# Kernel tuning notes

Measured on AMD Instinct MI355X. Metric: run time of the kernel, lower is better.

## Reference

```python
import jax, jax.numpy as jnp
import numpy as np

H = 7        # num attention heads (must divide D=791)
TOP_NUM = 2  # hard-coded in select(attn_tensor, 2)


def setup_inputs() -> dict:
    key = jax.random.key(0)
    ks = jax.random.split(key, 7)
    B, N, D = 32, 512, 791  # D = 2*hidden_dim + 23, hidden_dim=384
    s = 1.0 / np.sqrt(D)
    return {
        "fuse_feature": jax.random.normal(ks[0], (B, N, D), jnp.float32),
        "Wq": jax.random.normal(ks[1], (D, D), jnp.float32) * s,
        "bq": jax.random.normal(ks[2], (D,), jnp.float32) * 0.01,
        "Wk": jax.random.normal(ks[3], (D, D), jnp.float32) * s,
        "bk": jax.random.normal(ks[4], (D,), jnp.float32) * 0.01,
        "W_gc": jax.random.normal(ks[5], (D, D), jnp.float32) * s,
        "b_gc": jax.random.normal(ks[6], (D,), jnp.float32) * 0.01,
    }


def _select(mat, top_num):
    """Faithful jax version of select(): per-batch top-k threshold,
    symmetrize (mask + mask^T), then fill diagonal with 1."""
    B, N, _ = mat.shape
    flat = mat.reshape(B, N * N)
    kth = jax.lax.top_k(flat, top_num)[0][:, -1]          # [B]
    m = (flat >= kth[:, None]).astype(mat.dtype).reshape(B, N, N)
    adj = m + jnp.swapaxes(m, -2, -1)                     # values in {0,1,2}
    eye = jnp.eye(N, dtype=bool)
    return jnp.where(eye[None], jnp.asarray(1.0, mat.dtype), adj)


def reference(fuse_feature, Wq, bq, Wk, bk, W_gc, b_gc):
    B, N, D = fuse_feature.shape
    dk = D // H

    # score_mask: positions where fuse @ fuse^T == 0 (padding detector)
    gram = jnp.einsum("bnd,bmd->bnm", fuse_feature, fuse_feature)
    score_mask = (gram == 0)[:, None]                     # [B,1,N,N]

    # multi-head attention probabilities (eval mode: no dropout)
    q = (fuse_feature @ Wq + bq).reshape(B, N, H, dk).transpose(0, 2, 1, 3)
    k = (fuse_feature @ Wk + bk).reshape(B, N, H, dk).transpose(0, 2, 1, 3)
    scores = jnp.einsum("bhnd,bhmd->bhnm", q, k) / jnp.sqrt(jnp.asarray(dk, q.dtype))
    scores = jnp.where(score_mask, -1e9, scores)
    valid = (~score_mask[..., 0:1]).astype(scores.dtype)  # [B,1,N,1]
    p_attn = jax.nn.softmax(scores, axis=-1) * valid

    attn = p_attn.sum(axis=1)                             # [B,N,N]
    att_adj = _select(attn, TOP_NUM) * attn

    # GraphConvolution (kg_gc): adj @ (x W) / (rowsum(adj)+1) + b, then relu
    hidden = fuse_feature @ W_gc
    denom = att_adj.sum(axis=2, keepdims=True) + 1.0
    out = jnp.einsum("bnm,bmd->bnd", att_adj, hidden) / denom + b_gc
    return jax.nn.relu(out)
```

## Files before the change

kernel.cpp:

```cpp
#include <hip/hip_runtime.h>

#define B_  32
#define N_  512
#define D_  791
#define H_  7
#define DK_ 113
#define M_  (B_*N_)
#define KP_ 800
#define DP_ 896
#define NKT 25

typedef __attribute__((ext_vector_type(8))) short bf16x8;
typedef __attribute__((ext_vector_type(4))) float f32x4;

__device__ __forceinline__ ushort f2bf_rn(float x) {
    uint u = __float_as_uint(x);
    uint r = (u + 0x7FFFu + ((u >> 16) & 1u)) >> 16;
    return (ushort)r;
}
__device__ __forceinline__ float bf2f(ushort h) {
    return __uint_as_float(((uint)h) << 16);
}
__device__ __forceinline__ void split_bf16(float x, ushort& h, ushort& l) {
    h = f2bf_rn(x);
    l = f2bf_rn(x - bf2f(h));
}

__device__ __forceinline__ void gload16(const void* g, void* l) {
    __builtin_amdgcn_global_load_lds(
        (const __attribute__((address_space(1))) void*)g,
        (__attribute__((address_space(3))) void*)l, 16, 0, 0);
}

__global__ __launch_bounds__(256)
void splitX_kernel(const float* __restrict__ X, ushort* __restrict__ Xh,
                   ushort* __restrict__ Xl)
{
    int g = blockIdx.x * 256 + threadIdx.x;
    if (g >= M_ * 100) return;
    int row = g / 100, grp = g % 100;
    int k0 = grp * 8;
    float v[8];
    if (k0 + 8 <= D_) {
        const float* p = X + (size_t)row * D_ + k0;
        #pragma unroll
        for (int i = 0; i < 8; ++i) v[i] = p[i];
    } else {
        #pragma unroll
        for (int i = 0; i < 8; ++i) {
            int k = k0 + i;
            v[i] = (k < D_) ? X[(size_t)row * D_ + k] : 0.f;
        }
    }
    bf16x8 hv, lv;
    #pragma unroll
    for (int i = 0; i < 8; ++i) {
        ushort h, l; split_bf16(v[i], h, l);
        hv[i] = (short)h; lv[i] = (short)l;
    }
    *(bf16x8*)&Xh[(size_t)row * KP_ + k0] = hv;
    *(bf16x8*)&Xl[(size_t)row * KP_ + k0] = lv;
}

__global__ __launch_bounds__(256)
void castWt_kernel(const float* __restrict__ W0, const float* __restrict__ W1,
                   const float* __restrict__ W2,
                   ushort* __restrict__ B0h, ushort* __restrict__ B0l,
                   ushort* __restrict__ B1h, ushort* __restrict__ B1l,
                   ushort* __restrict__ B2h, ushort* __restrict__ B2l)
{
    __shared__ ushort WsH[32][34], WsL[32][34];
    const int pc0 = blockIdx.x * 32;
    const int k0  = blockIdx.y * 32;
    const int w   = blockIdx.z;
    const float* W = (w == 0) ? W0 : (w == 1) ? W1 : W2;
    ushort* Bh = (w == 0) ? B0h : (w == 1) ? B1h : B2h;
    ushort* Bl = (w == 0) ? B0l : (w == 1) ? B1l : B2l;
    const int tx = threadIdx.x & 31, ty = threadIdx.x >> 5;

    #pragma unroll
    for (int r = 0; r < 4; ++r) {
        int kl = ty + 8 * r, k = k0 + kl;
        int pc = pc0 + tx;
        int src;
        if (w == 2) src = (pc < D_) ? pc : -1;
        else { int hh = pc >> 7, off = pc & 127; src = (off < DK_) ? hh * DK_ + off : -1; }
        float v = (src >= 0 && k < D_) ? W[(size_t)k * D_ + src] : 0.f;
        ushort h, l; split_bf16(v, h, l);
        WsH[tx][kl] = h; WsL[tx][kl] = l;
    }
    __syncthreads();
    #pragma unroll
    for (int r = 0; r < 4; ++r) {
        int pcl = ty + 8 * r, pc = pc0 + pcl;
        int k = k0 + tx;
        Bh[(size_t)pc * KP_ + k] = WsH[pcl][tx];
        Bl[(size_t)pc * KP_ + k] = WsL[pcl][tx];
    }
}

#define STAGE_PAIR(dH, dL, srcH, srcL, rowBase, kk0)                         \
    {                                                                        \
        _Pragma("unroll")                                                    \
        for (int j = 0; j < 2; ++j) {                                        \
            int c  = t + 256 * j;                                            \
            int r  = c >> 2, q = c & 3;                                      \
            int qs = q ^ ((r >> 1) & 3);                                     \
            size_t go = (size_t)(rowBase + r) * KP_ + (kk0) + qs * 8;        \
            int lofs = ((t & 192) + 256 * j) * 8;                            \
            gload16(&srcH[go], (dH) + lofs);                                 \
            gload16(&srcL[go], (dL) + lofs);                                 \
        }                                                                    \
    }
#define STAGE_ONE(dH, srcH, rowBase, kk0)                                    \
    {                                                                        \
        _Pragma("unroll")                                                    \
        for (int j = 0; j < 2; ++j) {                                        \
            int c  = t + 256 * j;                                            \
            int r  = c >> 2, q = c & 3;                                      \
            int qs = q ^ ((r >> 1) & 3);                                     \
            size_t go = (size_t)(rowBase + r) * KP_ + (kk0) + qs * 8;        \
            int lofs = ((t & 192) + 256 * j) * 8;                            \
            gload16(&srcH[go], (dH) + lofs);                                 \
        }                                                                    \
    }

struct GemmAcc { f32x4 a[4][4]; };

__global__ __launch_bounds__(256)
void gemm_qk_kernel(const ushort* __restrict__ Xh, const ushort* __restrict__ Xl,
                    const ushort* __restrict__ Bqh, const ushort* __restrict__ Bql,
                    const ushort* __restrict__ Bkh, const ushort* __restrict__ Bkl,
                    const float* __restrict__ bq, const float* __restrict__ bk,
                    ushort* __restrict__ Qh, ushort* __restrict__ Ql,
                    ushort* __restrict__ Kh, ushort* __restrict__ Kl)
{
    __shared__ ushort AsH[2][128*32], AsL[2][128*32];
    __shared__ ushort BsH[2][128*32], BsL[2][128*32];
    const int flat = blockIdx.x + 14 * blockIdx.y;
    const int nid  = (flat & 7) * 224 + (flat >> 3);
    const int by = nid / 14, bx = nid % 14;
    const int w = bx / 7, ct = bx % 7;
    const int row0 = by * 128, col0 = ct * 128;
    const ushort* Bh = w ? Bkh : Bqh;
    const ushort* Bl = w ? Bkl : Bql;
    const float* bias = w ? bk : bq;
    ushort* Ch = w ? Kh : Qh;
    ushort* Cl = w ? Kl : Ql;

    const int t = threadIdx.x, lane = t & 63, wid = t >> 6;
    const int wr = wid >> 1, wc = wid & 1;
    const int fr = lane & 15, kq = lane >> 4;

    GemmAcc acc;
    #pragma unroll
    for (int m = 0; m < 4; ++m)
        #pragma unroll
        for (int n = 0; n < 4; ++n) acc.a[m][n] = (f32x4){0.f,0.f,0.f,0.f};

    STAGE_PAIR(AsH[0], AsL[0], Xh, Xl, row0, 0)
    STAGE_PAIR(BsH[0], BsL[0], Bh, Bl, col0, 0)
    __syncthreads();

    for (int kt = 0; kt < NKT; ++kt) {
        const int cur = kt & 1;
        if (kt + 1 < NKT) {
            STAGE_PAIR(AsH[cur^1], AsL[cur^1], Xh, Xl, row0, (kt+1)*32)
            STAGE_PAIR(BsH[cur^1], BsL[cur^1], Bh, Bl, col0, (kt+1)*32)
        }
        bf16x8 aH[4], aL[4], bH[4], bL[4];
        #pragma unroll
        for (int m = 0; m < 4; ++m) {
            int r = wr * 64 + m * 16 + fr;
            int off = r * 32 + (kq ^ ((r >> 1) & 3)) * 8;
            aH[m] = *(const bf16x8*)&AsH[cur][off];
            aL[m] = *(const bf16x8*)&AsL[cur][off];
        }
        #pragma unroll
        for (int n = 0; n < 4; ++n) {
            int c = wc * 64 + n * 16 + fr;
            int off = c * 32 + (kq ^ ((c >> 1) & 3)) * 8;
            bH[n] = *(const bf16x8*)&BsH[cur][off];
            bL[n] = *(const bf16x8*)&BsL[cur][off];
        }
        #pragma unroll
        for (int m = 0; m < 4; ++m)
            #pragma unroll
            for (int n = 0; n < 4; ++n) {
                acc.a[m][n] = __builtin_amdgcn_mfma_f32_16x16x32_bf16(aH[m], bH[n], acc.a[m][n], 0, 0, 0);
                acc.a[m][n] = __builtin_amdgcn_mfma_f32_16x16x32_bf16(aH[m], bL[n], acc.a[m][n], 0, 0, 0);
                acc.a[m][n] = __builtin_amdgcn_mfma_f32_16x16x32_bf16(aL[m], bH[n], acc.a[m][n], 0, 0, 0);
            }
        __syncthreads();
    }

    const int orow = kq * 4;
    #pragma unroll
    for (int n = 0; n < 4; ++n) {
        int pc = col0 + wc * 64 + n * 16 + fr;
        int hh = pc >> 7, off = pc & 127;
        float bb = (off < DK_) ? bias[hh * DK_ + off] : 0.f;
        #pragma unroll
        for (int m = 0; m < 4; ++m)
            #pragma unroll
            for (int j = 0; j < 4; ++j) {
                int gr = row0 + wr * 64 + m * 16 + orow + j;
                float v = acc.a[m][n][j] + bb;
                ushort h, l; split_bf16(v, h, l);
                Ch[(size_t)gr * DP_ + pc] = h;
                Cl[(size_t)gr * DP_ + pc] = l;
            }
    }
}

__global__ __launch_bounds__(256)
void gemm_hd_kernel(const ushort* __restrict__ Xh,
                    const ushort* __restrict__ Bgh, const ushort* __restrict__ Bgl,
                    float* __restrict__ Cf)
{
    __shared__ ushort AsH[2][128*32];
    __shared__ ushort BsH[2][128*32], BsL[2][128*32];
    const int flat = blockIdx.x + 7 * blockIdx.y;
    const int nid  = (flat & 7) * 112 + (flat >> 3);
    const int by = nid / 7, bx = nid % 7;
    const int row0 = by * 128, col0 = bx * 128;

    const int t = threadIdx.x, lane = t & 63, wid = t >> 6;
    const int wr = wid >> 1, wc = wid & 1;
    const int fr = lane & 15, kq = lane >> 4;

    GemmAcc acc;
    #pragma unroll
    for (int m = 0; m < 4; ++m)
        #pragma unroll
        for (int n = 0; n < 4; ++n) acc.a[m][n] = (f32x4){0.f,0.f,0.f,0.f};

    STAGE_ONE(AsH[0], Xh, row0, 0)
    STAGE_PAIR(BsH[0], BsL[0], Bgh, Bgl, col0, 0)
    __syncthreads();

    for (int kt = 0; kt < NKT; ++kt) {
        const int cur = kt & 1;
        if (kt + 1 < NKT) {
            STAGE_ONE(AsH[cur^1], Xh, row0, (kt+1)*32)
            STAGE_PAIR(BsH[cur^1], BsL[cur^1], Bgh, Bgl, col0, (kt+1)*32)
        }
        bf16x8 aH[4], bH[4], bL[4];
        #pragma unroll
        for (int m = 0; m < 4; ++m) {
            int r = wr * 64 + m * 16 + fr;
            int off = r * 32 + (kq ^ ((r >> 1) & 3)) * 8;
            aH[m] = *(const bf16x8*)&AsH[cur][off];
        }
        #pragma unroll
        for (int n = 0; n < 4; ++n) {
            int c = wc * 64 + n * 16 + fr;
            int off = c * 32 + (kq ^ ((c >> 1) & 3)) * 8;
            bH[n] = *(const bf16x8*)&BsH[cur][off];
            bL[n] = *(const bf16x8*)&BsL[cur][off];
        }
        #pragma unroll
        for (int m = 0; m < 4; ++m)
            #pragma unroll
            for (int n = 0; n < 4; ++n) {
                acc.a[m][n] = __builtin_amdgcn_mfma_f32_16x16x32_bf16(aH[m], bH[n], acc.a[m][n], 0, 0, 0);
                acc.a[m][n] = __builtin_amdgcn_mfma_f32_16x16x32_bf16(aH[m], bL[n], acc.a[m][n], 0, 0, 0);
            }
        __syncthreads();
    }

    const int orow = kq * 4;
    #pragma unroll
    for (int n = 0; n < 4; ++n) {
        int gc = col0 + wc * 64 + n * 16 + fr;
        if (gc < D_) {
            #pragma unroll
            for (int m = 0; m < 4; ++m)
                #pragma unroll
                for (int j = 0; j < 4; ++j) {
                    int gr = row0 + wr * 64 + m * 16 + orow + j;
                    Cf[(size_t)gr * D_ + gc] = acc.a[m][n][j];
                }
        }
    }
}

__global__ __launch_bounds__(256, 2)
void attn_mfma(const ushort* __restrict__ Qh, const ushort* __restrict__ Ql,
               const ushort* __restrict__ Kh, const ushort* __restrict__ Kl,
               float* __restrict__ attn, float* __restrict__ diag,
               float* __restrict__ candv, int* __restrict__ candi)
{
    __shared__ ushort KsH[512*32];
    __shared__ ushort KsL[512*32];
    __shared__ float redA[4][32];
    __shared__ float redB[4][32];
    __shared__ float wv[8]; __shared__ int wi[8];

    const int t = threadIdx.x, lane = t & 63, w = t >> 6;
    const int bid = blockIdx.x;
    const int swz = (bid & 7) * 64 + (bid >> 3);
    const int b = swz >> 4, r0 = (swz & 15) * 32;
    const int fr = lane & 15, kg = (lane >> 4) * 8;
    const float scale = 0.09407208683f;

    f32x4 accA[2][8];
    #pragma unroll
    for (int m = 0; m < 2; ++m)
        #pragma unroll
        for (int n = 0; n < 8; ++n) accA[m][n] = (f32x4){0.f,0.f,0.f,0.f};

    for (int h = 0; h < H_; ++h) {
        f32x4 S[2][8];
        #pragma unroll
        for (int m = 0; m < 2; ++m)
            #pragma unroll
            for (int n = 0; n < 8; ++n) S[m][n] = (f32x4){0.f,0.f,0.f,0.f};

        #pragma unroll
        for (int kk = 0; kk < 4; ++kk) {
            bf16x8 qH[2], qL[2];
            #pragma unroll
            for (int m = 0; m < 2; ++m) {
                size_t qo = (size_t)(b * N_ + r0 + m * 16 + fr) * DP_ + h * 128 + kk * 32 + kg;
                qH[m] = *(const bf16x8*)&Qh[qo];
                qL[m] = *(const bf16x8*)&Ql[qo];
            }
            #pragma unroll
            for (int i = 0; i < 8; ++i) {
                int g = t + 256 * i;
                int key = g >> 2, c8 = (g & 3) * 8;
                size_t go = (size_t)(b * N_ + key) * DP_ + h * 128 + kk * 32 + c8;
                int lo = key * 32 + (c8 ^ ((key & 3) * 8));
                *(bf16x8*)&KsH[lo] = *(const bf16x8*)&Kh[go];
                *(bf16x8*)&KsL[lo] = *(const bf16x8*)&Kl[go];
            }
            __syncthreads();
            #pragma unroll
            for (int n = 0; n < 8; ++n) {
                int key = w * 128 + n * 16 + fr;
                int lo = key * 32 + (kg ^ ((key & 3) * 8));
                bf16x8 bH = *(const bf16x8*)&KsH[lo];
                bf16x8 bL = *(const bf16x8*)&KsL[lo];
                #pragma unroll
                for (int m = 0; m < 2; ++m) {
                    S[m][n] = __builtin_amdgcn_mfma_f32_16x16x32_bf16(qH[m], bH, S[m][n], 0, 0, 0);
                    S[m][n] = __builtin_amdgcn_mfma_f32_16x16x32_bf16(qH[m], bL, S[m][n], 0, 0, 0);
                    S[m][n] = __builtin_amdgcn_mfma_f32_16x16x32_bf16(qL[m], bH, S[m][n], 0, 0, 0);
                }
            }
            __syncthreads();
        }

        float fm[2][4];
        #pragma unroll
        for (int m = 0; m < 2; ++m)
            #pragma unroll
            for (int j = 0; j < 4; ++j) {
                float mx = -1e30f;
                #pragma unroll
                for (int n = 0; n < 8; ++n) {
                    S[m][n][j] *= scale;
                    mx = fmaxf(mx, S[m][n][j]);
                }
                #pragma unroll
                for (int d = 1; d < 16; d <<= 1) mx = fmaxf(mx, __shfl_xor(mx, d));
                fm[m][j] = mx;
            }
        if ((lane & 15) == 0) {
            #pragma unroll
            for (int m = 0; m < 2; ++m)
                #pragma unroll
                for (int j = 0; j < 4; ++j)
                    redA[w][m * 16 + (lane >> 4) * 4 + j] = fm[m][j];
        }
        __syncthreads();
        #pragma unroll
        for (int m = 0; m < 2; ++m)
            #pragma unroll
            for (int j = 0; j < 4; ++j) {
                int q = m * 16 + (lane >> 4) * 4 + j;
                float mx = redA[0][q];
                mx = fmaxf(mx, redA[1][q]);
                mx = fmaxf(mx, redA[2][q]);
                mx = fmaxf(mx, redA[3][q]);
                fm[m][j] = mx;
            }
        float sm[2][4];
        #pragma unroll
        for (int m = 0; m < 2; ++m)
            #pragma unroll
            for (int j = 0; j < 4; ++j) {
                float s = 0.f;
                #pragma unroll
                for (int n = 0; n < 8; ++n) {
                    float e = __expf(S[m][n][j] - fm[m][j]);
                    S[m][n][j] = e; s += e;
                }
                #pragma unroll
                for (int d = 1; d < 16; d <<= 1) s += __shfl_xor(s, d);
                sm[m][j] = s;
            }
        if ((lane & 15) == 0) {
            #pragma unroll
            for (int m = 0; m < 2; ++m)
                #pragma unroll
                for (int j = 0; j < 4; ++j)
                    redB[w][m * 16 + (lane >> 4) * 4 + j] = sm[m][j];
        }
        __syncthreads();
        #pragma unroll
        for (int m = 0; m < 2; ++m)
            #pragma unroll
            for (int j = 0; j < 4; ++j) {
                int q = m * 16 + (lane >> 4) * 4 + j;
                float s = redB[0][q] + redB[1][q] + redB[2][q] + redB[3][q];
                float rinv = 1.f / s;
                #pragma unroll
                for (int n = 0; n < 8; ++n)
                    accA[m][n][j] += S[m][n][j] * rinv;
            }
        __syncthreads();
    }

    float* ab = attn + (size_t)b * N_ * N_;
    #pragma unroll
    for (int m = 0; m < 2; ++m)
        #pragma unroll
        for (int j = 0; j < 4; ++j) {
            int row = r0 + m * 16 + (lane >> 4) * 4 + j;
            float* ar = ab + (size_t)row * N_;
            #pragma unroll
            for (int n = 0; n < 8; ++n) {
                int col = w * 128 + n * 16 + fr;
                ar[col] = accA[m][n][j];
                if (col == row) diag[b * N_ + row] = accA[m][n][j];
            }
        }

    float v1 = -1e30f, v2 = -1e30f; int i1 = 0, i2 = 0;
    #pragma unroll
    for (int m = 0; m < 2; ++m)
        #pragma unroll
        for (int n = 0; n < 8; ++n)
            #pragma unroll
            for (int j = 0; j < 4; ++j) {
                float v = accA[m][n][j];
                int row = r0 + m * 16 + (lane >> 4) * 4 + j;
                int col = w * 128 + n * 16 + fr;
                int idx = row * N_ + col;
                if (v > v1)      { v2 = v1; i2 = i1; v1 = v; i1 = idx; }
                else if (v > v2) { v2 = v;  i2 = idx; }
            }
    #pragma unroll
    for (int d = 1; d < 64; d <<= 1) {
        float ov1 = __shfl_xor(v1, d); int oi1 = __shfl_xor(i1, d);
        float ov2 = __shfl_xor(v2, d); int oi2 = __shfl_xor(i2, d);
        if (ov1 > v1)      { v2 = v1; i2 = i1; v1 = ov1; i1 = oi1; }
        else if (ov1 > v2) { v2 = ov1; i2 = oi1; }
        if (ov2 > v1)      { v2 = v1; i2 = i1; v1 = ov2; i1 = oi2; }
        else if (ov2 > v2) { v2 = ov2; i2 = oi2; }
    }
    if (lane == 0) { wv[w*2] = v1; wi[w*2] = i1; wv[w*2+1] = v2; wi[w*2+1] = i2; }
    __syncthreads();
    if (t == 0) {
        float g1 = -1e30f, g2 = -1e30f; int gi1 = 0, gi2 = 0;
        for (int e = 0; e < 8; ++e) {
            float v = wv[e]; int ii = wi[e];
            if (v > g1)      { g2 = g1; gi2 = gi1; g1 = v; gi1 = ii; }
            else if (v > g2) { g2 = v; gi2 = ii; }
        }
        int cb = (b * 16 + (swz & 15)) * 2;
        candv[cb] = g1; candi[cb] = gi1;
        candv[cb+1] = g2; candi[cb+1] = gi2;
    }
}

__global__ __launch_bounds__(64)
void merge_kernel(const float* __restrict__ attn, const float* __restrict__ candv,
                  const int* __restrict__ candi,
                  int* __restrict__ tidx, float* __restrict__ tval)
{
    const int b = blockIdx.x;
    if (threadIdx.x != 0) return;
    const float* ab = attn + (size_t)b * N_ * N_;
    float v1 = -1e30f, v2 = -1e30f; int i1 = 0, i2 = 0;
    for (int s = 0; s < 32; ++s) {
        float v = candv[b * 32 + s]; int ii = candi[b * 32 + s];
        if (v > v1)      { v2 = v1; i2 = i1; v1 = v; i1 = ii; }
        else if (v > v2) { v2 = v; i2 = ii; }
    }
    int r1 = i1 / N_, c1 = i1 % N_;
    int r2 = i2 / N_, c2 = i2 % N_;
    tidx[b*4+0] = r1; tidx[b*4+1] = c1; tidx[b*4+2] = r2; tidx[b*4+3] = c2;
    tval[b*4+0] = ab[(size_t)r1 * N_ + c1];
    tval[b*4+1] = ab[(size_t)c1 * N_ + r1];
    tval[b*4+2] = ab[(size_t)r2 * N_ + c2];
    tval[b*4+3] = ab[(size_t)c2 * N_ + r2];
}

__global__ __launch_bounds__(256)
void out_kernel(const float* __restrict__ Hd, const float* __restrict__ diag,
                const int* __restrict__ tidx, const float* __restrict__ tval,
                const float* __restrict__ bgc, float* __restrict__ out)
{
    const int bn = blockIdx.x;
    const int b = bn >> 9, n = bn & 511;
    const int t = threadIdx.x;

    const int r1 = tidx[b*4+0], c1 = tidx[b*4+1];
    const int r2 = tidx[b*4+2], c2 = tidx[b*4+3];

    int   mc[4]; float mv[4]; int nc = 0;
    if (r1 != c1) {
        if (n == r1) { mc[nc] = c1; mv[nc] = tval[b*4+0]; ++nc; }
        if (n == c1) { mc[nc] = r1; mv[nc] = tval[b*4+1]; ++nc; }
    }
    if (r2 != c2) {
        if (n == r2) { mc[nc] = c2; mv[nc] = tval[b*4+2]; ++nc; }
        if (n == c2) { mc[nc] = r2; mv[nc] = tval[b*4+3]; ++nc; }
    }
    const float dg = diag[bn];
    float denom = dg + 1.0f;
    for (int i = 0; i < nc; ++i) denom += mv[i];
    const float rd = 1.f / denom;

    const float* hn = Hd + (size_t)bn * D_;
    for (int d = t; d < D_; d += 256) {
        float acc = dg * hn[d];
        for (int i = 0; i < nc; ++i)
            acc += mv[i] * Hd[(size_t)(b * N_ + mc[i]) * D_ + d];
        float o = acc * rd + bgc[d];
        out[(size_t)bn * D_ + d] = fmaxf(o, 0.f);
    }
}

extern "C" void kernel_launch(void* const* d_in, const int* in_sizes, int n_in,
                              void* d_out, int out_size, void* d_ws, size_t ws_size,
                              hipStream_t stream)
{
    const float* X   = (const float*)d_in[0];
    const float* Wq  = (const float*)d_in[1];
    const float* bq  = (const float*)d_in[2];
    const float* Wk  = (const float*)d_in[3];
    const float* bk  = (const float*)d_in[4];
    const float* Wgc = (const float*)d_in[5];
    const float* bgc = (const float*)d_in[6];
    float* out = (float*)d_out;

    ushort* wsu = (ushort*)d_ws;
    const size_t MDP = (size_t)M_ * DP_;
    const size_t MKP = (size_t)M_ * KP_;
    ushort* Qh = wsu;
    ushort* Ql = wsu + MDP;
    ushort* Kh = wsu + 2 * MDP;
    ushort* Kl = wsu + 3 * MDP;
    ushort* Bt = wsu + 4 * MDP;
    const size_t BSZ = (size_t)DP_ * KP_;
    ushort* Bqh = Bt;            ushort* Bql = Bt + BSZ;
    ushort* Bkh = Bt + 2 * BSZ;  ushort* Bkl = Bt + 3 * BSZ;
    ushort* Bgh = Bt + 4 * BSZ;  ushort* Bgl = Bt + 5 * BSZ;
    ushort* Xh  = Bt + 6 * BSZ;
    float* diag  = (float*)(Xh + MKP);
    int*   tidx  = (int*)(diag + M_);
    float* tval  = (float*)(tidx + 128);
    float* candv = tval + 128;
    int*   candi = (int*)(candv + 1024);
    ushort* Xl  = (ushort*)d_out;
    float* Hd   = (float*)d_ws;
    float* attn = out;

    hipLaunchKernelGGL(splitX_kernel, dim3((M_ * 100 + 255) / 256), dim3(256), 0, stream,
                       X, Xh, Xl);
    hipLaunchKernelGGL(castWt_kernel, dim3(DP_ / 32, NKT, 3), dim3(256), 0, stream,
                       Wq, Wk, Wgc, Bqh, Bql, Bkh, Bkl, Bgh, Bgl);

    hipLaunchKernelGGL(gemm_qk_kernel, dim3(14, 128), dim3(256), 0, stream,
                       Xh, Xl, Bqh, Bql, Bkh, Bkl, bq, bk, Qh, Ql, Kh, Kl);

    hipLaunchKernelGGL(attn_mfma, dim3(512), dim3(256), 0, stream,
                       Qh, Ql, Kh, Kl, attn, diag, candv, candi);
    hipLaunchKernelGGL(merge_kernel, dim3(B_), dim3(64), 0, stream,
                       attn, candv, candi, tidx, tval);

    hipLaunchKernelGGL(gemm_hd_kernel, dim3(7, 128), dim3(256), 0, stream,
                       Xh, Bgh, Bgl, Hd);

    hipLaunchKernelGGL(out_kernel, dim3(M_), dim3(256), 0, stream,
                       Hd, diag, tidx, tval, bgc, out);
}
```

Before: 600.4 us.

## Single-buffer GEMM LDS staging and use direct global-to-LDS loads for K in attention

Both projection GEMMs drop double-buffered LDS and now load, sync and compute each K tile in turn, which halves LDS use and may raise occupancy. The cost is that global loads no longer overlap the MFMA work. The attention kernel replaces register-staged K tile loads with gload16 direct-to-LDS loads using a permuted swizzle, issued before the Q register loads. This cuts VGPR traffic in the K staging. The GEMM loop as shown has no trailing barrier before the next overwrite unless one is kept after the MFMAs, so it relies on the existing end-of-loop sync.

Measured after the change: 512.2 us. 14.7% less time.

```diff
diff --git a/kernel.cpp b/kernel.cpp
--- a/kernel.cpp
+++ b/kernel.cpp
@@ -135,8 +135,7 @@
                     ushort* __restrict__ Qh, ushort* __restrict__ Ql,
                     ushort* __restrict__ Kh, ushort* __restrict__ Kl)
 {
-    __shared__ ushort AsH[2][128*32], AsL[2][128*32];
-    __shared__ ushort BsH[2][128*32], BsL[2][128*32];
+    __shared__ ushort AsH[128*32], AsL[128*32], BsH[128*32], BsL[128*32];
     const int flat = blockIdx.x + 14 * blockIdx.y;
     const int nid  = (flat & 7) * 224 + (flat >> 3);
     const int by = nid / 14, bx = nid % 14;
@@ -158,30 +157,25 @@
         #pragma unroll
         for (int n = 0; n < 4; ++n) acc.a[m][n] = (f32x4){0.f,0.f,0.f,0.f};
 
-    STAGE_PAIR(AsH[0], AsL[0], Xh, Xl, row0, 0)
-    STAGE_PAIR(BsH[0], BsL[0], Bh, Bl, col0, 0)
-    __syncthreads();
-
-    for (int kt = 0; kt < NKT; ++kt) {
-        const int cur = kt & 1;
-        if (kt + 1 < NKT) {
-            STAGE_PAIR(AsH[cur^1], AsL[cur^1], Xh, Xl, row0, (kt+1)*32)
-            STAGE_PAIR(BsH[cur^1], BsL[cur^1], Bh, Bl, col0, (kt+1)*32)
-        }
+    for (int k0 = 0; k0 < KP_; k0 += 32) {
+        STAGE_PAIR(AsH, AsL, Xh, Xl, row0, k0)
+        STAGE_PAIR(BsH, BsL, Bh, Bl, col0, k0)
+        __syncthreads();
+
         bf16x8 aH[4], aL[4], bH[4], bL[4];
         #pragma unroll
         for (int m = 0; m < 4; ++m) {
             int r = wr * 64 + m * 16 + fr;
             int off = r * 32 + (kq ^ ((r >> 1) & 3)) * 8;
-            aH[m] = *(const bf16x8*)&AsH[cur][off];
-            aL[m] = *(const bf16x8*)&AsL[cur][off];
+            aH[m] = *(const bf16x8*)&AsH[off];
+            aL[m] = *(const bf16x8*)&AsL[off];
         }
         #pragma unroll
         for (int n = 0; n < 4; ++n) {
             int c = wc * 64 + n * 16 + fr;
             int off = c * 32 + (kq ^ ((c >> 1) & 3)) * 8;
-            bH[n] = *(const bf16x8*)&BsH[cur][off];
-            bL[n] = *(const bf16x8*)&BsL[cur][off];
+            bH[n] = *(const bf16x8*)&BsH[off];
+            bL[n] = *(const bf16x8*)&BsL[off];
         }
         #pragma unroll
         for (int m = 0; m < 4; ++m)
@@ -218,8 +212,7 @@
                     const ushort* __restrict__ Bgh, const ushort* __restrict__ Bgl,
                     float* __restrict__ Cf)
 {
-    __shared__ ushort AsH[2][128*32];
-    __shared__ ushort BsH[2][128*32], BsL[2][128*32];
+    __shared__ ushort AsH[128*32], BsH[128*32], BsL[128*32];
     const int flat = blockIdx.x + 7 * blockIdx.y;
     const int nid  = (flat & 7) * 112 + (flat >> 3);
     const int by = nid / 7, bx = nid % 7;
@@ -235,29 +228,24 @@
         #pragma unroll
         for (int n = 0; n < 4; ++n) acc.a[m][n] = (f32x4){0.f,0.f,0.f,0.f};
 
-    STAGE_ONE(AsH[0], Xh, row0, 0)
-    STAGE_PAIR(BsH[0], BsL[0], Bgh, Bgl, col0, 0)
-    __syncthreads();
-
-    for (int kt = 0; kt < NKT; ++kt) {
-        const int cur = kt & 1;
-        if (kt + 1 < NKT) {
-            STAGE_ONE(AsH[cur^1], Xh, row0, (kt+1)*32)
-            STAGE_PAIR(BsH[cur^1], BsL[cur^1], Bgh, Bgl, col0, (kt+1)*32)
-        }
+    for (int k0 = 0; k0 < KP_; k0 += 32) {
+        STAGE_ONE(AsH, Xh, row0, k0)
+        STAGE_PAIR(BsH, BsL, Bgh, Bgl, col0, k0)
+        __syncthreads();
+
         bf16x8 aH[4], bH[4], bL[4];
         #pragma unroll
         for (int m = 0; m < 4; ++m) {
             int r = wr * 64 + m * 16 + fr;
             int off = r * 32 + (kq ^ ((r >> 1) & 3)) * 8;
-            aH[m] = *(const bf16x8*)&AsH[cur][off];
+            aH[m] = *(const bf16x8*)&AsH[off];
         }
         #pragma unroll
         for (int n = 0; n < 4; ++n) {
             int c = wc * 64 + n * 16 + fr;
             int off = c * 32 + (kq ^ ((c >> 1) & 3)) * 8;
-            bH[n] = *(const bf16x8*)&BsH[cur][off];
-            bL[n] = *(const bf16x8*)&BsL[cur][off];
+            bH[n] = *(const bf16x8*)&BsH[off];
+            bL[n] = *(const bf16x8*)&BsL[off];
         }
         #pragma unroll
         for (int m = 0; m < 4; ++m)
@@ -301,7 +289,7 @@
     const int bid = blockIdx.x;
     const int swz = (bid & 7) * 64 + (bid >> 3);
     const int b = swz >> 4, r0 = (swz & 15) * 32;
-    const int fr = lane & 15, kg = (lane >> 4) * 8;
+    const int fr = lane & 15, kq = lane >> 4, kg = kq * 8;
     const float scale = 0.09407208683f;
 
     f32x4 accA[2][8];
@@ -319,6 +307,16 @@
 
         #pragma unroll
         for (int kk = 0; kk < 4; ++kk) {
+            #pragma unroll
+            for (int i = 0; i < 8; ++i) {
+                int g = t + 256 * i;
+                int key = g >> 2, cl = g & 3;
+                int cs = cl ^ (key & 3);
+                size_t go = (size_t)(b * N_ + key) * DP_ + h * 128 + kk * 32 + cs * 8;
+                int lofs = ((t & 192) + 256 * i) * 8;
+                gload16(&Kh[go], KsH + lofs);
+                gload16(&Kl[go], KsL + lofs);
+            }
             bf16x8 qH[2], qL[2];
             #pragma unroll
             for (int m = 0; m < 2; ++m) {
@@ -326,20 +324,11 @@
                 qH[m] = *(const bf16x8*)&Qh[qo];
                 qL[m] = *(const bf16x8*)&Ql[qo];
             }
-            #pragma unroll
-            for (int i = 0; i < 8; ++i) {
-                int g = t + 256 * i;
-                int key = g >> 2, c8 = (g & 3) * 8;
-                size_t go = (size_t)(b * N_ + key) * DP_ + h * 128 + kk * 32 + c8;
-                int lo = key * 32 + (c8 ^ ((key & 3) * 8));
-                *(bf16x8*)&KsH[lo] = *(const bf16x8*)&Kh[go];
-                *(bf16x8*)&KsL[lo] = *(const bf16x8*)&Kl[go];
-            }
             __syncthreads();
             #pragma unroll
             for (int n = 0; n < 8; ++n) {
                 int key = w * 128 + n * 16 + fr;
-                int lo = key * 32 + (kg ^ ((key & 3) * 8));
+                int lo = key * 32 + ((kq ^ (key & 3)) * 8);
                 bf16x8 bH = *(const bf16x8*)&KsH[lo];
                 bf16x8 bL = *(const bf16x8*)&KsL[lo];
                 #pragma unroll
@@ -372,14 +361,14 @@
             for (int m = 0; m < 2; ++m)
                 #pragma unroll
                 for (int j = 0; j < 4; ++j)
-                    redA[w][m * 16 + (lane >> 4) * 4 + j] = fm[m][j];
+                    redA[w][m * 16 + kq * 4 + j] = fm[m][j];
         }
         __syncthreads();
         #pragma unroll
         for (int m = 0; m < 2; ++m)
             #pragma unroll
             for (int j = 0; j < 4; ++j) {
-                int q = m * 16 + (lane >> 4) * 4 + j;
+                int q = m * 16 + kq * 4 + j;
                 float mx = redA[0][q];
                 mx = fmaxf(mx, redA[1][q]);
                 mx = fmaxf(mx, redA[2][q]);
@@ -406,14 +395,14 @@
             for (int m = 0; m < 2; ++m)
                 #pragma unroll
                 for (int j = 0; j < 4; ++j)
-                    redB[w][m * 16 + (lane >> 4) * 4 + j] = sm[m][j];
+                    redB[w][m * 16 + kq * 4 + j] = sm[m][j];
         }
         __syncthreads();
         #pragma unroll
         for (int m = 0; m < 2; ++m)
             #pragma unroll
             for (int j = 0; j < 4; ++j) {
-                int q = m * 16 + (lane >> 4) * 4 + j;
+                int q = m * 16 + kq * 4 + j;
                 float s = redB[0][q] + redB[1][q] + redB[2][q] + redB[3][q];
                 float rinv = 1.f / s;
                 #pragma unroll
@@ -428,7 +417,7 @@
     for (int m = 0; m < 2; ++m)
         #pragma unroll
         for (int j = 0; j < 4; ++j) {
-            int row = r0 + m * 16 + (lane >> 4) * 4 + j;
+            int row = r0 + m * 16 + kq * 4 + j;
             float* ar = ab + (size_t)row * N_;
             #pragma unroll
             for (int n = 0; n < 8; ++n) {
@@ -446,7 +435,7 @@
             #pragma unroll
             for (int j = 0; j < 4; ++j) {
                 float v = accA[m][n][j];
-                int row = r0 + m * 16 + (lane >> 4) * 4 + j;
+                int row = r0 + m * 16 + kq * 4 + j;
                 int col = w * 128 + n * 16 + fr;
                 int idx = row * N_ + col;
                 if (v > v1)      { v2 = v1; i2 = i1; v1 = v; i1 = idx; }
```
